# Optimization experiments

Hardware: AMD Instinct MI355X
Metric: run time of the kernel (lower is better)

## Reference

```python
import jax, jax.numpy as jnp
import numpy as np

N_NODES = 100000
N_EDGES = 1000000
D_FEAT = 64
N_FILTER = 64
N_CLASSES = 16


def gcn_norm(edge_idx, n):
    """Add self-loops and compute symmetric normalization D^-1/2 (A+I) D^-1/2."""
    loop = jnp.arange(n, dtype=edge_idx.dtype)
    src = jnp.concatenate([edge_idx[0], loop])  # [E+N]
    dst = jnp.concatenate([edge_idx[1], loop])  # [E+N]
    w = jnp.ones(src.shape[0], dtype=jnp.float32)
    deg = jax.ops.segment_sum(w, dst, num_segments=n)  # in-degree incl. self-loop
    dinv = jnp.where(deg > 0, jax.lax.rsqrt(deg), 0.0)
    norm = dinv[src] * w * dinv[dst]  # [E+N]
    return src, dst, norm


def gcn_conv(x, W, b, src, dst, norm, n):
    h = x @ W                                   # [n, f] dense transform first (f <= d)
    msg = h[src] * norm[:, None]                # gather + scale  [E+N, f]
    out = jax.ops.segment_sum(msg, dst, num_segments=n)  # scatter-add  [n, f]
    return out + b


def setup_inputs() -> dict:
    key = jax.random.key(0)
    k1, k2, k3, k4 = jax.random.split(key, 4)
    X = jax.random.normal(k1, (N_NODES, D_FEAT), dtype=jnp.float32)
    edge_idx = jax.random.randint(k2, (2, N_EDGES), 0, N_NODES, dtype=jnp.int64)
    W1 = jax.random.normal(k3, (D_FEAT, N_FILTER), dtype=jnp.float32) * 0.05
    b1 = jnp.zeros((N_FILTER,), dtype=jnp.float32)
    W2 = jax.random.normal(k4, (N_FILTER, N_CLASSES), dtype=jnp.float32) * 0.05
    b2 = jnp.zeros((N_CLASSES,), dtype=jnp.float32)
    return {"X": X, "edge_idx": edge_idx, "W1": W1, "b1": b1, "W2": W2, "b2": b2}


def reference(X, edge_idx, W1, b1, W2, b2):
    n = X.shape[0]
    src, dst, norm = gcn_norm(edge_idx, n)
    x = gcn_conv(X, W1, b1, src, dst, norm, n)
    x = jax.nn.relu(x)
    # dropout p=0 -> identity
    x = gcn_conv(x, W2, b2, src, dst, norm, n)
    return x  # raw logits; pred_layer is not applied in the torch forward
```

## Files before the change

kernel.cpp:

```cpp
#include <hip/hip_runtime.h>
#include <hip/hip_bf16.h>


constexpr int N = 100000;
constexpr int E = 1000000;
constexpr int NB = (N + 511) / 512;
constexpr int CAP = 6144;
constexpr int CSTRIDE = 32;
constexpr int CHUNK = 4096;
constexpr int NBLK = (E + CHUNK - 1) / CHUNK;
constexpr int NPW = 6;
constexpr int NW = (N + NPW - 1) / NPW;
constexpr int NWBLK = (NW + 3) / 4;

__device__ __forceinline__ float bflo(unsigned u) { return __uint_as_float(u << 16); }
__device__ __forceinline__ float bfhi(unsigned u) { return __uint_as_float(u & 0xffff0000u); }

__global__ void k_bfill(const int* __restrict__ src, const int* __restrict__ dst,
                        int* __restrict__ cursor, int* __restrict__ bkt) {
    __shared__ int hist[256];
    __shared__ int lbase[256];
    __shared__ int gbase[256];
    __shared__ int lcur[256];
    __shared__ int stage[CHUNK];
    __shared__ unsigned char sbkt[CHUNK];
    int t = threadIdx.x;
    int e0 = blockIdx.x * CHUNK;
    int cnt = min(CHUNK, E - e0);

    hist[t] = 0;
    __syncthreads();
    for (int j = t; j < cnt; j += 256)
        atomicAdd(&hist[dst[e0 + j] >> 9], 1);
    __syncthreads();
    int h = hist[t];
    lbase[t] = h;
    __syncthreads();
    for (int off = 1; off < 256; off <<= 1) {
        int x = (t >= off) ? lbase[t - off] : 0;
        __syncthreads();
        lbase[t] += x;
        __syncthreads();
    }
    int excl = lbase[t] - h;
    __syncthreads();
    lbase[t] = excl;
    lcur[t] = 0;
    if (t < NB) gbase[t] = h ? atomicAdd(&cursor[t * CSTRIDE], h) : 0;
    __syncthreads();
    for (int j = t; j < cnt; j += 256) {
        int d = dst[e0 + j];
        int b = d >> 9;
        int pos = lbase[b] + atomicAdd(&lcur[b], 1);
        stage[pos] = ((d & 511) << 17) | src[e0 + j];
        sbkt[pos] = (unsigned char)b;
    }
    __syncthreads();
    for (int j = t; j < cnt; j += 256) {
        int b = sbkt[j];
        int gpos = gbase[b] + (j - lbase[b]);
        if (gpos < CAP) bkt[b * CAP + gpos] = stage[j];
    }
}

__global__ void k_bfine(const int* __restrict__ cursor, const int* __restrict__ bkt,
                        int* __restrict__ row_ptr, float* __restrict__ dinv,
                        int* __restrict__ csr_src) {
    __shared__ int sd[256];
    __shared__ int cnt[512];
    __shared__ int excl[512];
    __shared__ int s2[256];
    int b = blockIdx.x;
    int t = threadIdx.x;
    int c = (t < NB) ? cursor[t * CSTRIDE] : 0;
    sd[t] = c;
    __syncthreads();
    for (int off = 1; off < 256; off <<= 1) {
        int x = (t >= off) ? sd[t - off] : 0;
        __syncthreads();
        sd[t] += x;
        __syncthreads();
    }
    int m = cursor[b * CSTRIDE];
    int base = sd[b] - m;
    if (b == 0 && t == 0) row_ptr[N] = E;
    const int* bb = bkt + b * CAP;
    const int4* bb4 = (const int4*)bb;
    int m4 = m >> 2;
    cnt[t] = 0; cnt[t + 256] = 0;
    __syncthreads();
    for (int j = t; j < m4; j += 256) {
        int4 v = bb4[j];
        atomicAdd(&cnt[v.x >> 17], 1); atomicAdd(&cnt[v.y >> 17], 1);
        atomicAdd(&cnt[v.z >> 17], 1); atomicAdd(&cnt[v.w >> 17], 1);
    }
    for (int j = (m4 << 2) + t; j < m; j += 256) atomicAdd(&cnt[bb[j] >> 17], 1);
    __syncthreads();
    int pairSum = cnt[2 * t] + cnt[2 * t + 1];
    s2[t] = pairSum;
    __syncthreads();
    for (int off = 1; off < 256; off <<= 1) {
        int x = (t >= off) ? s2[t - off] : 0;
        __syncthreads();
        s2[t] += x;
        __syncthreads();
    }
    int exclPair = s2[t] - pairSum;
    excl[2 * t] = exclPair;
    excl[2 * t + 1] = exclPair + cnt[2 * t];
    __syncthreads();
#pragma unroll
    for (int hh = 0; hh < 2; ++hh) {
        int k = t + hh * 256;
        int node = b * 512 + k;
        if (node < N) {
            row_ptr[node] = base + excl[k];
            dinv[node] = rsqrtf((float)(cnt[k] + 1));
        }
    }
    __syncthreads();
    for (int j = t; j < m4; j += 256) {
        int4 v = bb4[j];
        int p0 = atomicAdd(&excl[v.x >> 17], 1); csr_src[base + p0] = v.x & 0x1FFFF;
        int p1 = atomicAdd(&excl[v.y >> 17], 1); csr_src[base + p1] = v.y & 0x1FFFF;
        int p2 = atomicAdd(&excl[v.z >> 17], 1); csr_src[base + p2] = v.z & 0x1FFFF;
        int p3 = atomicAdd(&excl[v.w >> 17], 1); csr_src[base + p3] = v.w & 0x1FFFF;
    }
    for (int j = (m4 << 2) + t; j < m; j += 256) {
        int v = bb[j];
        int p = atomicAdd(&excl[v >> 17], 1);
        csr_src[base + p] = v & 0x1FFFF;
    }
}

__global__ void k_gemm1(const float* __restrict__ X, const float* __restrict__ W1,
                        const float* __restrict__ dinv, __hip_bfloat16* __restrict__ h1s,
                        __hip_bfloat16* __restrict__ h2s) {
    __shared__ float sX[4][4][64];
    int t = threadIdx.x;
    int lane = t & 63;
    int w = t >> 6;
    int wid = (blockIdx.x * 256 + t) >> 6;
    if (blockIdx.x == 0) {
        if (t < 64) h1s[(size_t)N * 64 + t] = __float2bfloat16(0.f);
        if (t < 16) h2s[(size_t)N * 16 + t] = __float2bfloat16(0.f);
    }
    float w1[64];
#pragma unroll
    for (int k = 0; k < 64; ++k) w1[k] = W1[k * 64 + lane];
    for (int r4 = wid * 4; r4 < N; r4 += 4096 * 4) {
#pragma unroll
        for (int j = 0; j < 4; ++j) sX[w][j][lane] = X[(size_t)(r4 + j) * 64 + lane];
        __builtin_amdgcn_s_waitcnt(0);
#pragma unroll
        for (int j = 0; j < 4; ++j) {
            float acc = 0.f;
#pragma unroll
            for (int k = 0; k < 64; ++k) acc = fmaf(sX[w][j][k], w1[k], acc);
            acc *= dinv[r4 + j];
            float up = __shfl_xor(acc, 1);
            if (!(lane & 1)) {
                __hip_bfloat162 p;
                p.x = __float2bfloat16(acc);
                p.y = __float2bfloat16(up);
                *(__hip_bfloat162*)(h1s + (size_t)(r4 + j) * 64 + lane) = p;
            }
        }
    }
}

__global__ void k_layer12(const int* __restrict__ row_ptr, const int* __restrict__ csr_src,
                          const float* __restrict__ dinv, const __hip_bfloat16* __restrict__ h1s,
                          const float* __restrict__ b1, const float* __restrict__ W2,
                          __hip_bfloat16* __restrict__ h2s) {
    __shared__ float sy[4][8][72];
    int t = threadIdx.x;
    int lane = t & 63;
    int w = t >> 6;
    int g8 = lane >> 3;
    int qo = (lane & 7) << 4;
    int g16 = lane >> 4, c16 = lane & 15;
    int wid = blockIdx.x * 4 + w;
    int d0 = wid * NPW;
    if (d0 >= N) return;
    int dend = min(d0 + NPW, N);
    float w2[16];
#pragma unroll
    for (int j = 0; j < 16; ++j) w2[j] = W2[(g16 * 16 + j) * 16 + c16];
    float b1v = b1[lane];
    const char* Hb = (const char*)h1s;

    int rp0 = row_ptr[d0];
    for (int d = d0; d < dend; ++d) {
        int rp1 = row_ptr[d + 1];
        float dv = dinv[d];
        float a[8] = {0, 0, 0, 0, 0, 0, 0, 0};
        if (g8 == 0) {
            uint4 u = *(const uint4*)(Hb + (((unsigned)d << 7) | qo));
            a[0] = bflo(u.x); a[1] = bfhi(u.x); a[2] = bflo(u.y); a[3] = bfhi(u.y);
            a[4] = bflo(u.z); a[5] = bfhi(u.z); a[6] = bflo(u.w); a[7] = bfhi(u.w);
        }
        for (int base = rp0; base < rp1; base += 64) {
            int nloc = min(64, rp1 - base);
            int sidx = (lane < nloc) ? csr_src[base + lane] : N;
            int steps = (nloc + 15) >> 4;
            for (int j = 0; j < steps; ++j) {
                int b0 = (j << 4) | g8;
                int s0 = __shfl(sidx, b0);
                int s1 = __shfl(sidx, b0 | 8);
                uint4 u0 = *(const uint4*)(Hb + (((unsigned)s0 << 7) | qo));
                uint4 u1 = *(const uint4*)(Hb + (((unsigned)s1 << 7) | qo));
                a[0] += bflo(u0.x); a[1] += bfhi(u0.x); a[2] += bflo(u0.y); a[3] += bfhi(u0.y);
                a[4] += bflo(u0.z); a[5] += bfhi(u0.z); a[6] += bflo(u0.w); a[7] += bfhi(u0.w);
                a[0] += bflo(u1.x); a[1] += bfhi(u1.x); a[2] += bflo(u1.y); a[3] += bfhi(u1.y);
                a[4] += bflo(u1.z); a[5] += bfhi(u1.z); a[6] += bflo(u1.w); a[7] += bfhi(u1.w);
            }
        }
        rp0 = rp1;
        float* row = &sy[w][g8][(lane & 7) << 3];
        *(float4*)row = make_float4(a[0], a[1], a[2], a[3]);
        *(float4*)(row + 4) = make_float4(a[4], a[5], a[6], a[7]);
        __builtin_amdgcn_s_waitcnt(0);
        float ysum = sy[w][0][lane] + sy[w][1][lane] + sy[w][2][lane] + sy[w][3][lane]
                   + sy[w][4][lane] + sy[w][5][lane] + sy[w][6][lane] + sy[w][7][lane];
        float y = fmaxf(fmaf(dv, ysum, b1v), 0.f);
        float o = 0.f;
#pragma unroll
        for (int j = 0; j < 16; ++j) o = fmaf(__shfl(y, (lane & 48) | j), w2[j], o);
        o += __shfl_xor(o, 16);
        o += __shfl_xor(o, 32);
        o *= dv;
        float oup = __shfl_xor(o, 1);
        if (lane < 16 && !(lane & 1)) {
            __hip_bfloat162 p;
            p.x = __float2bfloat16(o);
            p.y = __float2bfloat16(oup);
            *(__hip_bfloat162*)(h2s + (size_t)d * 16 + lane) = p;
        }
    }
}

__global__ void k_gather2(const int* __restrict__ row_ptr, const int* __restrict__ csr_src,
                          const float* __restrict__ dinv, const __hip_bfloat16* __restrict__ h2s,
                          const float* __restrict__ b2, float* __restrict__ out) {
    int t = threadIdx.x;
    int lane = t & 63;
    int g4 = lane >> 2;
    int q2 = lane & 3;
    int qo = q2 << 3;
    int wid = blockIdx.x * 4 + (t >> 6);
    int d0 = wid * NPW;
    if (d0 >= N) return;
    int dend = min(d0 + NPW, N);
    float b2v[4];
#pragma unroll
    for (int k = 0; k < 4; ++k) b2v[k] = b2[q2 * 4 + k];
    const char* Hb = (const char*)h2s;

    int rp0 = row_ptr[d0];
    for (int d = d0; d < dend; ++d) {
        int rp1 = row_ptr[d + 1];
        float dv = dinv[d];
        float a[4] = {0, 0, 0, 0};
        if (g4 == 0) {
            uint2 u = *(const uint2*)(Hb + (((unsigned)d << 5) | qo));
            a[0] = bflo(u.x); a[1] = bfhi(u.x); a[2] = bflo(u.y); a[3] = bfhi(u.y);
        }
        for (int base = rp0; base < rp1; base += 64) {
            int nloc = min(64, rp1 - base);
            int sidx = (lane < nloc) ? csr_src[base + lane] : N;
            int steps = (nloc + 15) >> 4;
            for (int j = 0; j < steps; ++j) {
                int s = __shfl(sidx, (j << 4) | g4);
                uint2 u = *(const uint2*)(Hb + (((unsigned)s << 5) | qo));
                a[0] += bflo(u.x); a[1] += bfhi(u.x);
                a[2] += bflo(u.y); a[3] += bfhi(u.y);
            }
        }
        rp0 = rp1;
#pragma unroll
        for (int k = 0; k < 4; ++k) {
            a[k] += __shfl_xor(a[k], 4);
            a[k] += __shfl_xor(a[k], 8);
            a[k] += __shfl_xor(a[k], 16);
            a[k] += __shfl_xor(a[k], 32);
        }
        if (lane < 4) {
            float4 r;
            r.x = fmaf(dv, a[0], b2v[0]);
            r.y = fmaf(dv, a[1], b2v[1]);
            r.z = fmaf(dv, a[2], b2v[2]);
            r.w = fmaf(dv, a[3], b2v[3]);
            *(float4*)(out + (size_t)d * 16 + q2 * 4) = r;
        }
    }
}

extern "C" void kernel_launch(void* const* d_in, const int* in_sizes, int n_in,
                              void* d_out, int out_size, void* d_ws, size_t ws_size,
                              hipStream_t stream) {
    const float* X  = (const float*)d_in[0];
    const int*   ei = (const int*)d_in[1];
    const float* W1 = (const float*)d_in[2];
    const float* b1 = (const float*)d_in[3];
    const float* W2 = (const float*)d_in[4];
    const float* b2 = (const float*)d_in[5];
    float* out = (float*)d_out;

    int* cursor  = (int*)d_ws;
    int* row_ptr = cursor + NB * CSTRIDE;
    int* bkt     = row_ptr + N + 4;
    int* csr_src = bkt + NB * CAP;
    float* dinv  = (float*)(csr_src + E);
    __hip_bfloat16* h1s = (__hip_bfloat16*)(dinv + N);
    __hip_bfloat16* h2s = h1s + (size_t)(N + 1) * 64;

    const int* src = ei;
    const int* dst = ei + E;

    hipMemsetAsync(cursor, 0, NB * CSTRIDE * sizeof(int), stream);
    k_bfill<<<NBLK, 256, 0, stream>>>(src, dst, cursor, bkt);
    k_bfine<<<NB, 256, 0, stream>>>(cursor, bkt, row_ptr, dinv, csr_src);
    k_gemm1<<<1024, 256, 0, stream>>>(X, W1, dinv, h1s, h2s);
    k_layer12<<<NWBLK, 256, 0, stream>>>(row_ptr, csr_src, dinv, h1s, b1, W2, h2s);
    k_gather2<<<NWBLK, 256, 0, stream>>>(row_ptr, csr_src, dinv, h2s, b2, out);
}
```

Measured before the change: 194.4 us.

## Interleave two destination nodes in gathers, prefetch X rows, use wave-shuffle scans

The two gather kernels now process two destination nodes at once, issuing both nodes' neighbor loads before accumulating. This raises memory-level parallelism for the latency-bound random gathers. The first GEMM register-prefetches the next X rows, computes four rows per k-loop, and waits only on LDS counters. The block-level Hillis-Steele shared-memory scans in the bucketing kernels are replaced with wave-shuffle scans, and the per-bucket base is computed with a masked reduction, cutting many barriers. Costs are higher register pressure and more complex control flow for odd tails.

```diff
diff --git a/kernel.cpp b/kernel.cpp
--- a/kernel.cpp
+++ b/kernel.cpp
@@ -16,12 +16,35 @@
 __device__ __forceinline__ float bflo(unsigned u) { return __uint_as_float(u << 16); }
 __device__ __forceinline__ float bfhi(unsigned u) { return __uint_as_float(u & 0xffff0000u); }
 
+__device__ __forceinline__ void wait_lgkm0() {
+    __builtin_amdgcn_s_waitcnt(0xc07f);
+    __builtin_amdgcn_sched_barrier(0);
+}
+
+__device__ __forceinline__ int inclScan256(int v, int t, int* ws) {
+    int lane = t & 63;
+#pragma unroll
+    for (int off = 1; off < 64; off <<= 1) {
+        int u = __shfl_up(v, off);
+        if (lane >= off) v += u;
+    }
+    if (lane == 63) ws[t >> 6] = v;
+    __syncthreads();
+    int wv = t >> 6;
+    int add = 0;
+    if (wv > 0) add += ws[0];
+    if (wv > 1) add += ws[1];
+    if (wv > 2) add += ws[2];
+    return v + add;
+}
+
 __global__ void k_bfill(const int* __restrict__ src, const int* __restrict__ dst,
                         int* __restrict__ cursor, int* __restrict__ bkt) {
     __shared__ int hist[256];
     __shared__ int lbase[256];
     __shared__ int gbase[256];
     __shared__ int lcur[256];
+    __shared__ int ws[4];
     __shared__ int stage[CHUNK];
     __shared__ unsigned char sbkt[CHUNK];
     int t = threadIdx.x;
@@ -34,17 +57,8 @@
         atomicAdd(&hist[dst[e0 + j] >> 9], 1);
     __syncthreads();
     int h = hist[t];
-    lbase[t] = h;
-    __syncthreads();
-    for (int off = 1; off < 256; off <<= 1) {
-        int x = (t >= off) ? lbase[t - off] : 0;
-        __syncthreads();
-        lbase[t] += x;
-        __syncthreads();
-    }
-    int excl = lbase[t] - h;
-    __syncthreads();
-    lbase[t] = excl;
+    int inc = inclScan256(h, t, ws);
+    lbase[t] = inc - h;
     lcur[t] = 0;
     if (t < NB) gbase[t] = h ? atomicAdd(&cursor[t * CSTRIDE], h) : 0;
     __syncthreads();
@@ -66,29 +80,24 @@
 __global__ void k_bfine(const int* __restrict__ cursor, const int* __restrict__ bkt,
                         int* __restrict__ row_ptr, float* __restrict__ dinv,
                         int* __restrict__ csr_src) {
-    __shared__ int sd[256];
     __shared__ int cnt[512];
     __shared__ int excl[512];
-    __shared__ int s2[256];
+    __shared__ int ws[4];
     int b = blockIdx.x;
     int t = threadIdx.x;
     int c = (t < NB) ? cursor[t * CSTRIDE] : 0;
-    sd[t] = c;
-    __syncthreads();
-    for (int off = 1; off < 256; off <<= 1) {
-        int x = (t >= off) ? sd[t - off] : 0;
-        __syncthreads();
-        sd[t] += x;
-        __syncthreads();
-    }
+    int mv = (t < b) ? c : 0;
+#pragma unroll
+    for (int off = 1; off < 64; off <<= 1) mv += __shfl_xor(mv, off);
+    if ((t & 63) == 0) ws[t >> 6] = mv;
+    cnt[t] = 0; cnt[t + 256] = 0;
+    __syncthreads();
+    int base = ws[0] + ws[1] + ws[2] + ws[3];
     int m = cursor[b * CSTRIDE];
-    int base = sd[b] - m;
     if (b == 0 && t == 0) row_ptr[N] = E;
     const int* bb = bkt + b * CAP;
     const int4* bb4 = (const int4*)bb;
     int m4 = m >> 2;
-    cnt[t] = 0; cnt[t + 256] = 0;
-    __syncthreads();
     for (int j = t; j < m4; j += 256) {
         int4 v = bb4[j];
         atomicAdd(&cnt[v.x >> 17], 1); atomicAdd(&cnt[v.y >> 17], 1);
@@ -97,15 +106,8 @@
     for (int j = (m4 << 2) + t; j < m; j += 256) atomicAdd(&cnt[bb[j] >> 17], 1);
     __syncthreads();
     int pairSum = cnt[2 * t] + cnt[2 * t + 1];
-    s2[t] = pairSum;
-    __syncthreads();
-    for (int off = 1; off < 256; off <<= 1) {
-        int x = (t >= off) ? s2[t - off] : 0;
-        __syncthreads();
-        s2[t] += x;
-        __syncthreads();
-    }
-    int exclPair = s2[t] - pairSum;
+    int inc2 = inclScan256(pairSum, t, ws);
+    int exclPair = inc2 - pairSum;
     excl[2 * t] = exclPair;
     excl[2 * t + 1] = exclPair + cnt[2 * t];
     __syncthreads();
@@ -148,24 +150,98 @@
     float w1[64];
 #pragma unroll
     for (int k = 0; k < 64; ++k) w1[k] = W1[k * 64 + lane];
-    for (int r4 = wid * 4; r4 < N; r4 += 4096 * 4) {
-#pragma unroll
-        for (int j = 0; j < 4; ++j) sX[w][j][lane] = X[(size_t)(r4 + j) * 64 + lane];
-        __builtin_amdgcn_s_waitcnt(0);
-#pragma unroll
-        for (int j = 0; j < 4; ++j) {
-            float acc = 0.f;
-#pragma unroll
-            for (int k = 0; k < 64; ++k) acc = fmaf(sX[w][j][k], w1[k], acc);
-            acc *= dinv[r4 + j];
-            float up = __shfl_xor(acc, 1);
-            if (!(lane & 1)) {
-                __hip_bfloat162 p;
-                p.x = __float2bfloat16(acc);
-                p.y = __float2bfloat16(up);
-                *(__hip_bfloat162*)(h1s + (size_t)(r4 + j) * 64 + lane) = p;
-            }
-        }
+    constexpr int STRIDE = 4096 * 4;
+    int r4 = wid * 4;
+    float x0 = X[(size_t)r4 * 64 + lane];
+    float x1 = X[(size_t)(r4 + 1) * 64 + lane];
+    float x2 = X[(size_t)(r4 + 2) * 64 + lane];
+    float x3 = X[(size_t)(r4 + 3) * 64 + lane];
+    for (; r4 < N; r4 += STRIDE) {
+        int rn = r4 + STRIDE;
+        float y0 = 0.f, y1 = 0.f, y2 = 0.f, y3 = 0.f;
+        if (rn < N) {
+            y0 = X[(size_t)rn * 64 + lane];
+            y1 = X[(size_t)(rn + 1) * 64 + lane];
+            y2 = X[(size_t)(rn + 2) * 64 + lane];
+            y3 = X[(size_t)(rn + 3) * 64 + lane];
+        }
+        float dv0 = dinv[r4], dv1 = dinv[r4 + 1], dv2 = dinv[r4 + 2], dv3 = dinv[r4 + 3];
+        sX[w][0][lane] = x0; sX[w][1][lane] = x1;
+        sX[w][2][lane] = x2; sX[w][3][lane] = x3;
+        wait_lgkm0();
+        float acc0 = 0.f, acc1 = 0.f, acc2 = 0.f, acc3 = 0.f;
+#pragma unroll
+        for (int k = 0; k < 64; ++k) {
+            float wk = w1[k];
+            acc0 = fmaf(sX[w][0][k], wk, acc0);
+            acc1 = fmaf(sX[w][1][k], wk, acc1);
+            acc2 = fmaf(sX[w][2][k], wk, acc2);
+            acc3 = fmaf(sX[w][3][k], wk, acc3);
+        }
+        acc0 *= dv0; acc1 *= dv1; acc2 *= dv2; acc3 *= dv3;
+        float up0 = __shfl_xor(acc0, 1);
+        float up1 = __shfl_xor(acc1, 1);
+        float up2 = __shfl_xor(acc2, 1);
+        float up3 = __shfl_xor(acc3, 1);
+        if (!(lane & 1)) {
+            __hip_bfloat162 p;
+            p.x = __float2bfloat16(acc0); p.y = __float2bfloat16(up0);
+            *(__hip_bfloat162*)(h1s + (size_t)r4 * 64 + lane) = p;
+            p.x = __float2bfloat16(acc1); p.y = __float2bfloat16(up1);
+            *(__hip_bfloat162*)(h1s + (size_t)(r4 + 1) * 64 + lane) = p;
+            p.x = __float2bfloat16(acc2); p.y = __float2bfloat16(up2);
+            *(__hip_bfloat162*)(h1s + (size_t)(r4 + 2) * 64 + lane) = p;
+            p.x = __float2bfloat16(acc3); p.y = __float2bfloat16(up3);
+            *(__hip_bfloat162*)(h1s + (size_t)(r4 + 3) * 64 + lane) = p;
+        }
+        x0 = y0; x1 = y1; x2 = y2; x3 = y3;
+    }
+}
+
+__device__ __forceinline__ void acc8(float a[8], uint4 u) {
+    a[0] += bflo(u.x); a[1] += bfhi(u.x); a[2] += bflo(u.y); a[3] += bfhi(u.y);
+    a[4] += bflo(u.z); a[5] += bfhi(u.z); a[6] += bflo(u.w); a[7] += bfhi(u.w);
+}
+
+__device__ __forceinline__ void gwin(float a[8], int base0, int rp1,
+                                     const int* __restrict__ csr_src, const char* Hb,
+                                     int lane, int g8, int qo) {
+    for (int base = base0; base < rp1; base += 64) {
+        int nloc = min(64, rp1 - base);
+        int sidx = (lane < nloc) ? csr_src[base + lane] : N;
+        int steps = (nloc + 15) >> 4;
+        for (int j = 0; j < steps; ++j) {
+            int b0 = (j << 4) | g8;
+            int s0 = __shfl(sidx, b0), s1 = __shfl(sidx, b0 | 8);
+            uint4 u0 = *(const uint4*)(Hb + (((unsigned)s0 << 7) | qo));
+            uint4 u1 = *(const uint4*)(Hb + (((unsigned)s1 << 7) | qo));
+            acc8(a, u0); acc8(a, u1);
+        }
+    }
+}
+
+__device__ __forceinline__ void mlp_store(const float a[8], float (*syp)[72], int lane, int g8,
+                                          const float* w2, float b1v, float dv, int dd,
+                                          __hip_bfloat16* __restrict__ h2s) {
+    float* rowp = &syp[g8][(lane & 7) << 3];
+    *(float4*)rowp = make_float4(a[0], a[1], a[2], a[3]);
+    *(float4*)(rowp + 4) = make_float4(a[4], a[5], a[6], a[7]);
+    wait_lgkm0();
+    float ysum = syp[0][lane] + syp[1][lane] + syp[2][lane] + syp[3][lane]
+               + syp[4][lane] + syp[5][lane] + syp[6][lane] + syp[7][lane];
+    float y = fmaxf(fmaf(dv, ysum, b1v), 0.f);
+    float o = 0.f;
+#pragma unroll
+    for (int j = 0; j < 16; ++j) o = fmaf(__shfl(y, (lane & 48) | j), w2[j], o);
+    o += __shfl_xor(o, 16);
+    o += __shfl_xor(o, 32);
+    o *= dv;
+    float oup = __shfl_xor(o, 1);
+    if (lane < 16 && !(lane & 1)) {
+        __hip_bfloat162 p;
+        p.x = __float2bfloat16(o);
+        p.y = __float2bfloat16(oup);
+        *(__hip_bfloat162*)(h2s + (size_t)dd * 16 + lane) = p;
     }
 }
 
@@ -173,7 +249,7 @@
                           const float* __restrict__ dinv, const __hip_bfloat16* __restrict__ h1s,
                           const float* __restrict__ b1, const float* __restrict__ W2,
                           __hip_bfloat16* __restrict__ h2s) {
-    __shared__ float sy[4][8][72];
+    __shared__ float sy[4][2][8][72];
     int t = threadIdx.x;
     int lane = t & 63;
     int w = t >> 6;
@@ -191,52 +267,90 @@
     const char* Hb = (const char*)h1s;
 
     int rp0 = row_ptr[d0];
-    for (int d = d0; d < dend; ++d) {
-        int rp1 = row_ptr[d + 1];
-        float dv = dinv[d];
-        float a[8] = {0, 0, 0, 0, 0, 0, 0, 0};
-        if (g8 == 0) {
-            uint4 u = *(const uint4*)(Hb + (((unsigned)d << 7) | qo));
-            a[0] = bflo(u.x); a[1] = bfhi(u.x); a[2] = bflo(u.y); a[3] = bfhi(u.y);
-            a[4] = bflo(u.z); a[5] = bfhi(u.z); a[6] = bflo(u.w); a[7] = bfhi(u.w);
-        }
-        for (int base = rp0; base < rp1; base += 64) {
-            int nloc = min(64, rp1 - base);
-            int sidx = (lane < nloc) ? csr_src[base + lane] : N;
-            int steps = (nloc + 15) >> 4;
-            for (int j = 0; j < steps; ++j) {
-                int b0 = (j << 4) | g8;
-                int s0 = __shfl(sidx, b0);
-                int s1 = __shfl(sidx, b0 | 8);
-                uint4 u0 = *(const uint4*)(Hb + (((unsigned)s0 << 7) | qo));
-                uint4 u1 = *(const uint4*)(Hb + (((unsigned)s1 << 7) | qo));
-                a[0] += bflo(u0.x); a[1] += bfhi(u0.x); a[2] += bflo(u0.y); a[3] += bfhi(u0.y);
-                a[4] += bflo(u0.z); a[5] += bfhi(u0.z); a[6] += bflo(u0.w); a[7] += bfhi(u0.w);
-                a[0] += bflo(u1.x); a[1] += bfhi(u1.x); a[2] += bflo(u1.y); a[3] += bfhi(u1.y);
-                a[4] += bflo(u1.z); a[5] += bfhi(u1.z); a[6] += bflo(u1.w); a[7] += bfhi(u1.w);
+    for (int d = d0; d < dend; d += 2) {
+        bool two = (d + 1 < dend);
+        int dB = two ? d + 1 : d;
+        int rpA0 = rp0;
+        int rpA1 = row_ptr[d + 1];
+        int rpB0 = rpA1;
+        int rpB1 = two ? row_ptr[d + 2] : rpA1;
+        rp0 = rpB1;
+        float dvA = dinv[d], dvB = dinv[dB];
+        float aA[8] = {0, 0, 0, 0, 0, 0, 0, 0};
+        float aB[8] = {0, 0, 0, 0, 0, 0, 0, 0};
+        bool selfok = (g8 == 0);
+        uint4 uSA, uSB;
+        if (selfok) {
+            uSA = *(const uint4*)(Hb + (((unsigned)d << 7) | qo));
+            uSB = *(const uint4*)(Hb + (((unsigned)dB << 7) | qo));
+        }
+        int nA = min(rpA1 - rpA0, 64);
+        int nB = min(rpB1 - rpB0, 64);
+        int sidxA = (lane < nA) ? csr_src[rpA0 + lane] : N;
+        int sidxB = (lane < nB) ? csr_src[rpB0 + lane] : N;
+        if (selfok) { acc8(aA, uSA); acc8(aB, uSB); }
+        int stepsA = (nA + 15) >> 4;
+        int stepsB = (nB + 15) >> 4;
+        int smax = max(stepsA, stepsB);
+        for (int j = 0; j < smax; ++j) {
+            int b0 = (j << 4) | g8;
+            bool da = j < stepsA, db = j < stepsB;
+            uint4 u0, u1, v0, v1;
+            if (da) {
+                int s0 = __shfl(sidxA, b0), s1 = __shfl(sidxA, b0 | 8);
+                u0 = *(const uint4*)(Hb + (((unsigned)s0 << 7) | qo));
+                u1 = *(const uint4*)(Hb + (((unsigned)s1 << 7) | qo));
             }
-        }
-        rp0 = rp1;
-        float* row = &sy[w][g8][(lane & 7) << 3];
-        *(float4*)row = make_float4(a[0], a[1], a[2], a[3]);
-        *(float4*)(row + 4) = make_float4(a[4], a[5], a[6], a[7]);
-        __builtin_amdgcn_s_waitcnt(0);
-        float ysum = sy[w][0][lane] + sy[w][1][lane] + sy[w][2][lane] + sy[w][3][lane]
-                   + sy[w][4][lane] + sy[w][5][lane] + sy[w][6][lane] + sy[w][7][lane];
-        float y = fmaxf(fmaf(dv, ysum, b1v), 0.f);
-        float o = 0.f;
-#pragma unroll
-        for (int j = 0; j < 16; ++j) o = fmaf(__shfl(y, (lane & 48) | j), w2[j], o);
-        o += __shfl_xor(o, 16);
-        o += __shfl_xor(o, 32);
-        o *= dv;
-        float oup = __shfl_xor(o, 1);
-        if (lane < 16 && !(lane & 1)) {
-            __hip_bfloat162 p;
-            p.x = __float2bfloat16(o);
-            p.y = __float2bfloat16(oup);
-            *(__hip_bfloat162*)(h2s + (size_t)d * 16 + lane) = p;
-        }
+            if (db) {
+                int s0 = __shfl(sidxB, b0), s1 = __shfl(sidxB, b0 | 8);
+                v0 = *(const uint4*)(Hb + (((unsigned)s0 << 7) | qo));
+                v1 = *(const uint4*)(Hb + (((unsigned)s1 << 7) | qo));
+            }
+            if (da) { acc8(aA, u0); acc8(aA, u1); }
+            if (db) { acc8(aB, v0); acc8(aB, v1); }
+        }
+        if (rpA0 + 64 < rpA1) gwin(aA, rpA0 + 64, rpA1, csr_src, Hb, lane, g8, qo);
+        if (rpB0 + 64 < rpB1) gwin(aB, rpB0 + 64, rpB1, csr_src, Hb, lane, g8, qo);
+        mlp_store(aA, sy[w][0], lane, g8, w2, b1v, dvA, d, h2s);
+        if (two) mlp_store(aB, sy[w][1], lane, g8, w2, b1v, dvB, dB, h2s);
+    }
+}
+
+__device__ __forceinline__ void acc4(float a[4], uint2 u) {
+    a[0] += bflo(u.x); a[1] += bfhi(u.x); a[2] += bflo(u.y); a[3] += bfhi(u.y);
+}
+
+__device__ __forceinline__ void g2win(float a[4], int base0, int rp1,
+                                      const int* __restrict__ csr_src, const char* Hb,
+                                      int lane, int g4, int qo) {
+    for (int base = base0; base < rp1; base += 64) {
+        int nloc = min(64, rp1 - base);
+        int sidx = (lane < nloc) ? csr_src[base + lane] : N;
+        int steps = (nloc + 15) >> 4;
+        for (int j = 0; j < steps; ++j) {
+            int s = __shfl(sidx, (j << 4) | g4);
+            uint2 u = *(const uint2*)(Hb + (((unsigned)s << 5) | qo));
+            acc4(a, u);
+        }
+    }
+}
+
+__device__ __forceinline__ void red_store(float a[4], int lane, int q2, const float* b2v,
+                                          float dv, int dd, float* __restrict__ out) {
+#pragma unroll
+    for (int k = 0; k < 4; ++k) {
+        a[k] += __shfl_xor(a[k], 4);
+        a[k] += __shfl_xor(a[k], 8);
+        a[k] += __shfl_xor(a[k], 16);
+        a[k] += __shfl_xor(a[k], 32);
+    }
+    if (lane < 4) {
+        float4 r;
+        r.x = fmaf(dv, a[0], b2v[0]);
+        r.y = fmaf(dv, a[1], b2v[1]);
+        r.z = fmaf(dv, a[2], b2v[2]);
+        r.w = fmaf(dv, a[3], b2v[3]);
+        *(float4*)(out + (size_t)dd * 16 + q2 * 4) = r;
     }
 }
 
@@ -258,41 +372,49 @@
     const char* Hb = (const char*)h2s;
 
     int rp0 = row_ptr[d0];
-    for (int d = d0; d < dend; ++d) {
-        int rp1 = row_ptr[d + 1];
-        float dv = dinv[d];
-        float a[4] = {0, 0, 0, 0};
-        if (g4 == 0) {
-            uint2 u = *(const uint2*)(Hb + (((unsigned)d << 5) | qo));
-            a[0] = bflo(u.x); a[1] = bfhi(u.x); a[2] = bflo(u.y); a[3] = bfhi(u.y);
-        }
-        for (int base = rp0; base < rp1; base += 64) {
-            int nloc = min(64, rp1 - base);
-            int sidx = (lane < nloc) ? csr_src[base + lane] : N;
-            int steps = (nloc + 15) >> 4;
-            for (int j = 0; j < steps; ++j) {
-                int s = __shfl(sidx, (j << 4) | g4);
-                uint2 u = *(const uint2*)(Hb + (((unsigned)s << 5) | qo));
-                a[0] += bflo(u.x); a[1] += bfhi(u.x);
-                a[2] += bflo(u.y); a[3] += bfhi(u.y);
+    for (int d = d0; d < dend; d += 2) {
+        bool two = (d + 1 < dend);
+        int dB = two ? d + 1 : d;
+        int rpA0 = rp0;
+        int rpA1 = row_ptr[d + 1];
+        int rpB0 = rpA1;
+        int rpB1 = two ? row_ptr[d + 2] : rpA1;
+        rp0 = rpB1;
+        float dvA = dinv[d], dvB = dinv[dB];
+        float aA[4] = {0, 0, 0, 0};
+        float aB[4] = {0, 0, 0, 0};
+        bool selfok = (g4 == 0);
+        uint2 uSA, uSB;
+        if (selfok) {
+            uSA = *(const uint2*)(Hb + (((unsigned)d << 5) | qo));
+            uSB = *(const uint2*)(Hb + (((unsigned)dB << 5) | qo));
+        }
+        int nA = min(rpA1 - rpA0, 64);
+        int nB = min(rpB1 - rpB0, 64);
+        int sidxA = (lane < nA) ? csr_src[rpA0 + lane] : N;
+        int sidxB = (lane < nB) ? csr_src[rpB0 + lane] : N;
+        if (selfok) { acc4(aA, uSA); acc4(aB, uSB); }
+        int stepsA = (nA + 15) >> 4;
+        int stepsB = (nB + 15) >> 4;
+        int smax = max(stepsA, stepsB);
+        for (int j = 0; j < smax; ++j) {
+            bool da = j < stepsA, db = j < stepsB;
+            uint2 uA, uB;
+            if (da) {
+                int s = __shfl(sidxA, (j << 4) | g4);
+                uA = *(const uint2*)(Hb + (((unsigned)s << 5) | qo));
             }
-        }
-        rp0 = rp1;
-#pragma unroll
-        for (int k = 0; k < 4; ++k) {
-            a[k] += __shfl_xor(a[k], 4);
-            a[k] += __shfl_xor(a[k], 8);
-            a[k] += __shfl_xor(a[k], 16);
-            a[k] += __shfl_xor(a[k], 32);
-        }
-        if (lane < 4) {
-            float4 r;
-            r.x = fmaf(dv, a[0], b2v[0]);
-            r.y = fmaf(dv, a[1], b2v[1]);
-            r.z = fmaf(dv, a[2], b2v[2]);
-            r.w = fmaf(dv, a[3], b2v[3]);
-            *(float4*)(out + (size_t)d * 16 + q2 * 4) = r;
-        }
+            if (db) {
+                int s = __shfl(sidxB, (j << 4) | g4);
+                uB = *(const uint2*)(Hb + (((unsigned)s << 5) | qo));
+            }
+            if (da) acc4(aA, uA);
+            if (db) acc4(aB, uB);
+        }
+        if (rpA0 + 64 < rpA1) g2win(aA, rpA0 + 64, rpA1, csr_src, Hb, lane, g4, qo);
+        if (rpB0 + 64 < rpB1) g2win(aB, rpB0 + 64, rpB1, csr_src, Hb, lane, g4, qo);
+        red_store(aA, lane, q2, b2v, dvA, d, out);
+        if (two) red_store(aB, lane, q2, b2v, dvB, dB, out);
     }
 }
 
```

After: 198.7 us. +2.2%, slower.

## Use wave-shuffle scans, 512-thread bucket kernels, and prefetch X in gemm1

Applied to the files above, without the earlier changes.

Replaces the shared-memory Hillis-Steele prefix scans in the bucket fill and fine-sort kernels with wave-level shuffle scans plus a small per-wave combine, removing many block barriers. The two CSR-building kernels now run 512 threads per block, and the fill kernel uses smaller edge chunks to launch more blocks. The first GEMM prefetches the next iteration's X rows into registers and computes four rows with independent accumulators. The full waitcnt is narrowed to an LDS-only wait with a scheduling barrier. Smaller chunks mean more global cursor atomics.

```diff
diff --git a/kernel.cpp b/kernel.cpp
--- a/kernel.cpp
+++ b/kernel.cpp
@@ -7,14 +7,20 @@
 constexpr int NB = (N + 511) / 512;
 constexpr int CAP = 6144;
 constexpr int CSTRIDE = 32;
-constexpr int CHUNK = 4096;
+constexpr int CHUNK = 2048;
 constexpr int NBLK = (E + CHUNK - 1) / CHUNK;
+constexpr int BT = 512;
 constexpr int NPW = 6;
 constexpr int NW = (N + NPW - 1) / NPW;
 constexpr int NWBLK = (NW + 3) / 4;
 
 __device__ __forceinline__ float bflo(unsigned u) { return __uint_as_float(u << 16); }
 __device__ __forceinline__ float bfhi(unsigned u) { return __uint_as_float(u & 0xffff0000u); }
+
+__device__ __forceinline__ void wait_lgkm0() {
+    __builtin_amdgcn_s_waitcnt(0xc07f);
+    __builtin_amdgcn_sched_barrier(0);
+}
 
 __global__ void k_bfill(const int* __restrict__ src, const int* __restrict__ dst,
                         int* __restrict__ cursor, int* __restrict__ bkt) {
@@ -22,33 +28,35 @@
     __shared__ int lbase[256];
     __shared__ int gbase[256];
     __shared__ int lcur[256];
+    __shared__ int ws[8];
     __shared__ int stage[CHUNK];
     __shared__ unsigned char sbkt[CHUNK];
     int t = threadIdx.x;
+    int lane = t & 63;
     int e0 = blockIdx.x * CHUNK;
     int cnt = min(CHUNK, E - e0);
 
-    hist[t] = 0;
-    __syncthreads();
-    for (int j = t; j < cnt; j += 256)
+    if (t < 256) hist[t] = 0;
+    __syncthreads();
+    for (int j = t; j < cnt; j += BT)
         atomicAdd(&hist[dst[e0 + j] >> 9], 1);
     __syncthreads();
-    int h = hist[t];
-    lbase[t] = h;
-    __syncthreads();
-    for (int off = 1; off < 256; off <<= 1) {
-        int x = (t >= off) ? lbase[t - off] : 0;
-        __syncthreads();
-        lbase[t] += x;
-        __syncthreads();
-    }
-    int excl = lbase[t] - h;
-    __syncthreads();
-    lbase[t] = excl;
-    lcur[t] = 0;
+    int h = (t < 256) ? hist[t] : 0;
+    int v = h;
+#pragma unroll
+    for (int off = 1; off < 64; off <<= 1) {
+        int u = __shfl_up(v, off);
+        if (lane >= off) v += u;
+    }
+    if (lane == 63) ws[t >> 6] = v;
+    __syncthreads();
+    int add = 0;
+    for (int i = 0; i < (t >> 6); ++i) add += ws[i];
+    int inc = v + add;
+    if (t < 256) { lbase[t] = inc - h; lcur[t] = 0; }
     if (t < NB) gbase[t] = h ? atomicAdd(&cursor[t * CSTRIDE], h) : 0;
     __syncthreads();
-    for (int j = t; j < cnt; j += 256) {
+    for (int j = t; j < cnt; j += BT) {
         int d = dst[e0 + j];
         int b = d >> 9;
         int pos = lbase[b] + atomicAdd(&lcur[b], 1);
@@ -56,7 +64,7 @@
         sbkt[pos] = (unsigned char)b;
     }
     __syncthreads();
-    for (int j = t; j < cnt; j += 256) {
+    for (int j = t; j < cnt; j += BT) {
         int b = sbkt[j];
         int gpos = gbase[b] + (j - lbase[b]);
         if (gpos < CAP) bkt[b * CAP + gpos] = stage[j];
@@ -66,70 +74,62 @@
 __global__ void k_bfine(const int* __restrict__ cursor, const int* __restrict__ bkt,
                         int* __restrict__ row_ptr, float* __restrict__ dinv,
                         int* __restrict__ csr_src) {
-    __shared__ int sd[256];
     __shared__ int cnt[512];
     __shared__ int excl[512];
-    __shared__ int s2[256];
+    __shared__ int ws[8];
     int b = blockIdx.x;
     int t = threadIdx.x;
+    int lane = t & 63;
     int c = (t < NB) ? cursor[t * CSTRIDE] : 0;
-    sd[t] = c;
-    __syncthreads();
-    for (int off = 1; off < 256; off <<= 1) {
-        int x = (t >= off) ? sd[t - off] : 0;
-        __syncthreads();
-        sd[t] += x;
-        __syncthreads();
-    }
+    int mv = (t < b) ? c : 0;
+#pragma unroll
+    for (int off = 1; off < 64; off <<= 1) mv += __shfl_xor(mv, off);
+    if (lane == 0) ws[t >> 6] = mv;
+    cnt[t] = 0;
+    __syncthreads();
+    int base = ws[0] + ws[1] + ws[2] + ws[3] + ws[4] + ws[5] + ws[6] + ws[7];
     int m = cursor[b * CSTRIDE];
-    int base = sd[b] - m;
     if (b == 0 && t == 0) row_ptr[N] = E;
     const int* bb = bkt + b * CAP;
     const int4* bb4 = (const int4*)bb;
     int m4 = m >> 2;
-    cnt[t] = 0; cnt[t + 256] = 0;
-    __syncthreads();
-    for (int j = t; j < m4; j += 256) {
+    for (int j = t; j < m4; j += BT) {
         int4 v = bb4[j];
         atomicAdd(&cnt[v.x >> 17], 1); atomicAdd(&cnt[v.y >> 17], 1);
         atomicAdd(&cnt[v.z >> 17], 1); atomicAdd(&cnt[v.w >> 17], 1);
     }
-    for (int j = (m4 << 2) + t; j < m; j += 256) atomicAdd(&cnt[bb[j] >> 17], 1);
-    __syncthreads();
-    int pairSum = cnt[2 * t] + cnt[2 * t + 1];
-    s2[t] = pairSum;
-    __syncthreads();
-    for (int off = 1; off < 256; off <<= 1) {
-        int x = (t >= off) ? s2[t - off] : 0;
-        __syncthreads();
-        s2[t] += x;
-        __syncthreads();
-    }
-    int exclPair = s2[t] - pairSum;
-    excl[2 * t] = exclPair;
-    excl[2 * t + 1] = exclPair + cnt[2 * t];
-    __syncthreads();
-#pragma unroll
-    for (int hh = 0; hh < 2; ++hh) {
-        int k = t + hh * 256;
-        int node = b * 512 + k;
-        if (node < N) {
-            row_ptr[node] = base + excl[k];
-            dinv[node] = rsqrtf((float)(cnt[k] + 1));
-        }
-    }
-    __syncthreads();
-    for (int j = t; j < m4; j += 256) {
-        int4 v = bb4[j];
-        int p0 = atomicAdd(&excl[v.x >> 17], 1); csr_src[base + p0] = v.x & 0x1FFFF;
-        int p1 = atomicAdd(&excl[v.y >> 17], 1); csr_src[base + p1] = v.y & 0x1FFFF;
-        int p2 = atomicAdd(&excl[v.z >> 17], 1); csr_src[base + p2] = v.z & 0x1FFFF;
-        int p3 = atomicAdd(&excl[v.w >> 17], 1); csr_src[base + p3] = v.w & 0x1FFFF;
-    }
-    for (int j = (m4 << 2) + t; j < m; j += 256) {
-        int v = bb[j];
-        int p = atomicAdd(&excl[v >> 17], 1);
-        csr_src[base + p] = v & 0x1FFFF;
+    for (int j = (m4 << 2) + t; j < m; j += BT) atomicAdd(&cnt[bb[j] >> 17], 1);
+    __syncthreads();
+    int h = cnt[t];
+    int v = h;
+#pragma unroll
+    for (int off = 1; off < 64; off <<= 1) {
+        int u = __shfl_up(v, off);
+        if (lane >= off) v += u;
+    }
+    if (lane == 63) ws[t >> 6] = v;
+    __syncthreads();
+    int add = 0;
+    for (int i = 0; i < (t >> 6); ++i) add += ws[i];
+    int ex = v + add - h;
+    excl[t] = ex;
+    int node = b * 512 + t;
+    if (node < N) {
+        row_ptr[node] = base + ex;
+        dinv[node] = rsqrtf((float)(h + 1));
+    }
+    __syncthreads();
+    for (int j = t; j < m4; j += BT) {
+        int4 v4 = bb4[j];
+        int p0 = atomicAdd(&excl[v4.x >> 17], 1); csr_src[base + p0] = v4.x & 0x1FFFF;
+        int p1 = atomicAdd(&excl[v4.y >> 17], 1); csr_src[base + p1] = v4.y & 0x1FFFF;
+        int p2 = atomicAdd(&excl[v4.z >> 17], 1); csr_src[base + p2] = v4.z & 0x1FFFF;
+        int p3 = atomicAdd(&excl[v4.w >> 17], 1); csr_src[base + p3] = v4.w & 0x1FFFF;
+    }
+    for (int j = (m4 << 2) + t; j < m; j += BT) {
+        int vv = bb[j];
+        int p = atomicAdd(&excl[vv >> 17], 1);
+        csr_src[base + p] = vv & 0x1FFFF;
     }
 }
 
@@ -148,24 +148,51 @@
     float w1[64];
 #pragma unroll
     for (int k = 0; k < 64; ++k) w1[k] = W1[k * 64 + lane];
-    for (int r4 = wid * 4; r4 < N; r4 += 4096 * 4) {
-#pragma unroll
-        for (int j = 0; j < 4; ++j) sX[w][j][lane] = X[(size_t)(r4 + j) * 64 + lane];
-        __builtin_amdgcn_s_waitcnt(0);
-#pragma unroll
-        for (int j = 0; j < 4; ++j) {
-            float acc = 0.f;
-#pragma unroll
-            for (int k = 0; k < 64; ++k) acc = fmaf(sX[w][j][k], w1[k], acc);
-            acc *= dinv[r4 + j];
-            float up = __shfl_xor(acc, 1);
-            if (!(lane & 1)) {
-                __hip_bfloat162 p;
-                p.x = __float2bfloat16(acc);
-                p.y = __float2bfloat16(up);
-                *(__hip_bfloat162*)(h1s + (size_t)(r4 + j) * 64 + lane) = p;
-            }
-        }
+    constexpr int STRIDE = 4096 * 4;
+    int r4 = wid * 4;
+    float x0 = X[(size_t)r4 * 64 + lane];
+    float x1 = X[(size_t)(r4 + 1) * 64 + lane];
+    float x2 = X[(size_t)(r4 + 2) * 64 + lane];
+    float x3 = X[(size_t)(r4 + 3) * 64 + lane];
+    for (; r4 < N; r4 += STRIDE) {
+        int rn = r4 + STRIDE;
+        float y0 = 0.f, y1 = 0.f, y2 = 0.f, y3 = 0.f;
+        if (rn < N) {
+            y0 = X[(size_t)rn * 64 + lane];
+            y1 = X[(size_t)(rn + 1) * 64 + lane];
+            y2 = X[(size_t)(rn + 2) * 64 + lane];
+            y3 = X[(size_t)(rn + 3) * 64 + lane];
+        }
+        float dv0 = dinv[r4], dv1 = dinv[r4 + 1], dv2 = dinv[r4 + 2], dv3 = dinv[r4 + 3];
+        sX[w][0][lane] = x0; sX[w][1][lane] = x1;
+        sX[w][2][lane] = x2; sX[w][3][lane] = x3;
+        wait_lgkm0();
+        float acc0 = 0.f, acc1 = 0.f, acc2 = 0.f, acc3 = 0.f;
+#pragma unroll
+        for (int k = 0; k < 64; ++k) {
+            float wk = w1[k];
+            acc0 = fmaf(sX[w][0][k], wk, acc0);
+            acc1 = fmaf(sX[w][1][k], wk, acc1);
+            acc2 = fmaf(sX[w][2][k], wk, acc2);
+            acc3 = fmaf(sX[w][3][k], wk, acc3);
+        }
+        acc0 *= dv0; acc1 *= dv1; acc2 *= dv2; acc3 *= dv3;
+        float up0 = __shfl_xor(acc0, 1);
+        float up1 = __shfl_xor(acc1, 1);
+        float up2 = __shfl_xor(acc2, 1);
+        float up3 = __shfl_xor(acc3, 1);
+        if (!(lane & 1)) {
+            __hip_bfloat162 p;
+            p.x = __float2bfloat16(acc0); p.y = __float2bfloat16(up0);
+            *(__hip_bfloat162*)(h1s + (size_t)r4 * 64 + lane) = p;
+            p.x = __float2bfloat16(acc1); p.y = __float2bfloat16(up1);
+            *(__hip_bfloat162*)(h1s + (size_t)(r4 + 1) * 64 + lane) = p;
+            p.x = __float2bfloat16(acc2); p.y = __float2bfloat16(up2);
+            *(__hip_bfloat162*)(h1s + (size_t)(r4 + 2) * 64 + lane) = p;
+            p.x = __float2bfloat16(acc3); p.y = __float2bfloat16(up3);
+            *(__hip_bfloat162*)(h1s + (size_t)(r4 + 3) * 64 + lane) = p;
+        }
+        x0 = y0; x1 = y1; x2 = y2; x3 = y3;
     }
 }
 
@@ -220,7 +247,7 @@
         float* row = &sy[w][g8][(lane & 7) << 3];
         *(float4*)row = make_float4(a[0], a[1], a[2], a[3]);
         *(float4*)(row + 4) = make_float4(a[4], a[5], a[6], a[7]);
-        __builtin_amdgcn_s_waitcnt(0);
+        wait_lgkm0();
         float ysum = sy[w][0][lane] + sy[w][1][lane] + sy[w][2][lane] + sy[w][3][lane]
                    + sy[w][4][lane] + sy[w][5][lane] + sy[w][6][lane] + sy[w][7][lane];
         float y = fmaxf(fmaf(dv, ysum, b1v), 0.f);
@@ -319,8 +346,8 @@
     const int* dst = ei + E;
 
     hipMemsetAsync(cursor, 0, NB * CSTRIDE * sizeof(int), stream);
-    k_bfill<<<NBLK, 256, 0, stream>>>(src, dst, cursor, bkt);
-    k_bfine<<<NB, 256, 0, stream>>>(cursor, bkt, row_ptr, dinv, csr_src);
+    k_bfill<<<NBLK, BT, 0, stream>>>(src, dst, cursor, bkt);
+    k_bfine<<<NB, BT, 0, stream>>>(cursor, bkt, row_ptr, dinv, csr_src);
     k_gemm1<<<1024, 256, 0, stream>>>(X, W1, dinv, h1s, h2s);
     k_layer12<<<NWBLK, 256, 0, stream>>>(row_ptr, csr_src, dinv, h1s, b1, W2, h2s);
     k_gather2<<<NWBLK, 256, 0, stream>>>(row_ptr, csr_src, dinv, h2s, b2, out);
```

New measurement: 186.8 us. 1.04x faster.
